# Performance work log

Hardware: AMD Instinct MI355X
Metric: run time of the kernel (lower is better)

Reference implementation:

```python
import jax, jax.numpy as jnp
import numpy as np

NUM_HEADS = 16
NUM_KV_HEADS = 4
HEAD_DIM = 128
HALF_DIM = HEAD_DIM // 2
LAMBDA_INIT = 0.8
LAMBDA_MIN = 0.0
LAMBDA_MAX = 1.0
CAUSAL = True
NORMALIZE_DIFF = True
NEG = -1.0e9


def setup_inputs() -> dict:
    key = jax.random.key(0)
    k1, k2, k3 = jax.random.split(key, 3)
    B, Sq, Sk = 1, 2048, 2048
    query = jax.random.normal(k1, (B, NUM_HEADS, Sq, HEAD_DIM), dtype=jnp.float32)
    key_t = jax.random.normal(k2, (B, NUM_KV_HEADS, Sk, HEAD_DIM), dtype=jnp.float32)
    value = jax.random.normal(k3, (B, NUM_KV_HEADS, Sk, HEAD_DIM), dtype=jnp.float32)
    return {"query": query, "key": key_t, "value": value}


def reference(query, key, value):
    scale = 1.0 / (HALF_DIM ** 0.5)
    lam = jnp.clip(jnp.float32(LAMBDA_INIT), LAMBDA_MIN, LAMBDA_MAX)
    # GQA: repeat KV heads to match query heads
    rep = NUM_HEADS // NUM_KV_HEADS
    k = jnp.repeat(key, rep, axis=1)    # [b,h,k,d]
    v = jnp.repeat(value, rep, axis=1)  # [b,h,k,d]
    q1, q2 = query[..., :HALF_DIM], query[..., HALF_DIM:]
    k1, k2 = k[..., :HALF_DIM], k[..., HALF_DIM:]
    scores1 = jnp.einsum('bhqd,bhkd->bhqk', q1, k1) * scale
    scores2 = jnp.einsum('bhqd,bhkd->bhqk', q2, k2) * scale
    if CAUSAL:
        Sq, Sk = query.shape[2], k.shape[2]
        mask = jnp.tril(jnp.ones((Sq, Sk), dtype=jnp.float32))  # lower-triangular causal
        scores1 = scores1 * mask + (1.0 - mask) * NEG
        scores2 = scores2 * mask + (1.0 - mask) * NEG
    attn1 = jax.nn.softmax(scores1, axis=-1)
    attn2 = jax.nn.softmax(scores2, axis=-1)
    diff_attn = attn1 - lam * attn2
    out = jnp.einsum('bhqk,bhkd->bhqd', diff_attn, v)
    if NORMALIZE_DIFF:
        out = out * (1.0 - LAMBDA_INIT)
    return out
```

## Files before the change

kernel.cpp:

```cpp
#include <hip/hip_runtime.h>

#define NUM_HEADS 16
#define HEAD_DIM  128
#define SEQ       2048
#define KT_STRIDE 8192

typedef __attribute__((ext_vector_type(8))) unsigned short us8;
typedef __attribute__((ext_vector_type(8))) __bf16 bf16x8;
typedef __attribute__((ext_vector_type(4))) float f32x4;
typedef __attribute__((ext_vector_type(16))) float f32x16;
typedef __attribute__((ext_vector_type(4))) unsigned u32x4;

static __device__ inline unsigned short f2bf(float x) {
    union { float f; unsigned u; } v; v.f = x;
    unsigned r = v.u + 0x7FFFu + ((v.u >> 16) & 1u);
    return (unsigned short)(r >> 16);
}
static __device__ inline unsigned pk2bf(float a, float b) {
    return (unsigned)f2bf(a) | ((unsigned)f2bf(b) << 16);
}
static __device__ inline float fast_exp2(float x) {
#if __has_builtin(__builtin_amdgcn_exp2f)
    return __builtin_amdgcn_exp2f(x);
#else
    return exp2f(x);
#endif
}
static __device__ inline unsigned pack_hi(unsigned clo, unsigned chi) {
#if __has_builtin(__builtin_amdgcn_perm)
    return __builtin_amdgcn_perm(chi, clo, 0x07060302u);
#else
    return (clo >> 16) | (chi & 0xffff0000u);
#endif
}
static __device__ inline f32x16 mfma32(us8 a, us8 b, f32x16 c) {
    return __builtin_amdgcn_mfma_f32_32x32x16_bf16(
        __builtin_bit_cast(bf16x8, a), __builtin_bit_cast(bf16x8, b), c, 0, 0, 0);
}

__global__ __launch_bounds__(256)
void prep_frag(const float* __restrict__ K, const float* __restrict__ V,
               unsigned short* __restrict__ KF, unsigned short* __restrict__ VF)
{
    const int bx  = (int)blockIdx.x, t = (int)threadIdx.x;
    const int which = bx & 1, kt = (bx >> 1) & 31, kvh = bx >> 6;
    __shared__ __align__(16) float Ls[64][132];

    const float* src = (which ? V : K) + ((size_t)kvh * SEQ + kt * 64) * HEAD_DIM;
    #pragma unroll
    for (int i = 0; i < 8; ++i) {
        const int idx = t + i * 256;
        const int r = idx >> 5, c4 = idx & 31;
        *(float4*)&Ls[r][c4 * 4] = *(const float4*)(src + (size_t)r * HEAD_DIM + c4 * 4);
    }
    __syncthreads();

    if (!which) {
        #pragma unroll
        for (int i = 0; i < 4; ++i) {
            const int c = t + i * 256;
            const int lane = c & 63, ds = (c >> 6) & 3, mat = (c >> 8) & 1, kh = c >> 9;
            const int H = lane >> 5;
            const int row = kh * 32 + (lane & 31);
            const int dim = mat * 64 + ds * 16 + H * 8;
            u32x4 pk;
            #pragma unroll
            for (int jj = 0; jj < 4; ++jj)
                pk[jj] = pk2bf(Ls[row][dim + 2*jj], Ls[row][dim + 2*jj + 1]);
            *(us8*)(KF + ((size_t)(kvh * 32 + kt) * 16 + kh * 8 + mat * 4 + ds) * 512 + lane * 8)
                = __builtin_bit_cast(us8, pk);
        }
    } else {
        #pragma unroll
        for (int i = 0; i < 4; ++i) {
            const int c = t + i * 256;
            const int lane = c & 63, db = (c >> 6) & 3, ks = (c >> 8) & 1, kh = c >> 9;
            const int H = lane >> 5;
            const int s0 = kh * 32 + ks * 16 + H * 8;
            const int d  = db * 32 + (lane & 31);
            u32x4 pk;
            #pragma unroll
            for (int jj = 0; jj < 4; ++jj)
                pk[jj] = pk2bf(Ls[s0 + 2*jj][d], Ls[s0 + 2*jj + 1][d]);
            *(us8*)(VF + ((size_t)(kvh * 32 + kt) * 16 + kh * 8 + ks * 4 + db) * 512 + lane * 8)
                = __builtin_bit_cast(us8, pk);
        }
    }
}

__global__ __launch_bounds__(256, 2)
void diff_attn_mfma10(const float* __restrict__ Q,
                      const unsigned short* __restrict__ KF,
                      const unsigned short* __restrict__ VF,
                      float* __restrict__ Out)
{
    __shared__ float cb[2][32][136];
    __shared__ float rsb[2][2][32];

    const int t   = (int)threadIdx.x;
    const int wv  = t >> 6;
    const int ln  = t & 63;
    const int mat = wv >> 1;
    const int kh  = wv & 1;
    const int q   = ln & 31;
    const int H   = ln >> 5;

    const int bx   = (int)blockIdx.x;
    const int h    = bx & 15;
    const int idx  = bx >> 4;
    const int qtA  = idx, qtB = 63 - idx;
    const int nktA = (qtA >> 1) + 1;
    const int kvh  = h >> 2;

    const unsigned short* kfb = KF + ((size_t)kvh * 32 * 16 + kh * 8 + mat * 4) * 512 + ln * 8;
    const unsigned short* vfb = VF + ((size_t)kvh * 32 * 16 + kh * 8) * 512 + ln * 8;

    const float qscale = 0.125f * 1.44269504088896340736f;

    us8 qhi[4];
    auto loadQ = [&](int q0c) {
        const float* qr = Q + ((size_t)h * SEQ + q0c + q) * HEAD_DIM + mat * 64;
        #pragma unroll
        for (int ds = 0; ds < 4; ++ds) {
            const int d0 = ds * 16 + H * 8;
            float x[8];
            *(float4*)&x[0] = *(const float4*)(qr + d0);
            *(float4*)&x[4] = *(const float4*)(qr + d0 + 4);
            us8 hi8;
            #pragma unroll
            for (int j = 0; j < 8; ++j) hi8[j] = f2bf(x[j] * qscale);
            qhi[ds] = hi8;
        }
    };

    f32x16 o[4];
    f32x4  rsv;

    auto epilogue = [&](int q0c) {
        __syncthreads();
        float rsc = (rsv[0] + rsv[1]) + (rsv[2] + rsv[3]);
        rsc += __shfl_xor(rsc, 32, 64);
        if (ln < 32) rsb[mat][kh][ln] = rsc;
        if (kh == 1) {
            #pragma unroll
            for (int db = 0; db < 4; ++db)
                #pragma unroll
                for (int i = 0; i < 4; ++i) {
                    float4 v = { o[db][i*4+0], o[db][i*4+1], o[db][i*4+2], o[db][i*4+3] };
                    *(float4*)&cb[mat][q][db * 32 + 8 * i + 4 * H] = v;
                }
        }
        __syncthreads();
        if (kh == 0) {
            const float l = rsb[mat][0][q] + rsb[mat][1][q];
            const float a = mat ? (0.16f / l) : (0.2f / l);
            #pragma unroll
            for (int db = 0; db < 4; ++db)
                #pragma unroll
                for (int i = 0; i < 4; ++i) {
                    float4 v = *(float4*)&cb[mat][q][db * 32 + 8 * i + 4 * H];
                    o[db][i*4+0] = (o[db][i*4+0] + v.x) * a;
                    o[db][i*4+1] = (o[db][i*4+1] + v.y) * a;
                    o[db][i*4+2] = (o[db][i*4+2] + v.z) * a;
                    o[db][i*4+3] = (o[db][i*4+3] + v.w) * a;
                }
            if (mat == 1) {
                #pragma unroll
                for (int db = 0; db < 4; ++db)
                    #pragma unroll
                    for (int i = 0; i < 4; ++i) {
                        float4 v = { o[db][i*4+0], o[db][i*4+1], o[db][i*4+2], o[db][i*4+3] };
                        *(float4*)&cb[1][q][db * 32 + 8 * i + 4 * H] = v;
                    }
            }
        }
        __syncthreads();
        if (wv == 0) {
            float* ob = Out + ((size_t)h * SEQ + q0c + q) * HEAD_DIM;
            #pragma unroll
            for (int db = 0; db < 4; ++db)
                #pragma unroll
                for (int i = 0; i < 4; ++i) {
                    float4 v = *(float4*)&cb[1][q][db * 32 + 8 * i + 4 * H];
                    float4 r;
                    r.x = o[db][i*4+0] - v.x;
                    r.y = o[db][i*4+1] - v.y;
                    r.z = o[db][i*4+2] - v.z;
                    r.w = o[db][i*4+3] - v.w;
                    *(float4*)(ob + db * 32 + 8 * i + 4 * H) = r;
                }
        }
    };

    auto run_seg = [&](int q0c, int nseg) {
        us8 kaA[4], kaB[4];

        auto body = [&](int j, us8 (&kaIn)[4], us8 (&kaOut)[4], f32x16& sIn, f32x16& sOut) {
            us8 va[8];
            {
                const unsigned short* vb = vfb + (size_t)j * KT_STRIDE;
                #pragma unroll
                for (int c = 0; c < 8; ++c) va[c] = *(const us8*)(vb + c * 512);
            }
            if (j + 2 < nseg) {
                const unsigned short* kb = kfb + (size_t)(j + 2) * KT_STRIDE;
                #pragma unroll
                for (int ds = 0; ds < 4; ++ds) kaOut[ds] = *(const us8*)(kb + ds * 512);
            }
            sOut = (f32x16)0.f;
            if (j + 1 < nseg) {
                #pragma unroll
                for (int ds = 0; ds < 4; ++ds) sOut = mfma32(kaIn[ds], qhi[ds], sOut);
            }
            unsigned c[16];
            if (j == nseg - 1) {
                const int kg0 = j * 64 + kh * 32 + 4 * H;
                const int qg  = q0c + q;
                #pragma unroll
                for (int r = 0; r < 16; ++r) {
                    const int kg = kg0 + (r & 3) + ((r >> 2) << 3);
                    float e = (kg <= qg) ? fast_exp2(sIn[r]) : 0.f;
                    c[r] = __builtin_bit_cast(unsigned, e);
                }
            } else {
                #pragma unroll
                for (int r = 0; r < 16; ++r)
                    c[r] = __builtin_bit_cast(unsigned, fast_exp2(sIn[r]));
            }
            #pragma unroll
            for (int ks = 0; ks < 2; ++ks) {
                const unsigned pA = pack_hi(c[8*ks+0], c[8*ks+1]);
                const unsigned pB = pack_hi(c[8*ks+2], c[8*ks+3]);
                const unsigned pC = pack_hi(c[8*ks+4], c[8*ks+5]);
                const unsigned pD = pack_hi(c[8*ks+6], c[8*ks+7]);
                rsv[0] += __builtin_bit_cast(float, pA << 16);
                rsv[1] += __builtin_bit_cast(float, pA & 0xffff0000u);
                rsv[2] += __builtin_bit_cast(float, pB << 16);
                rsv[3] += __builtin_bit_cast(float, pB & 0xffff0000u);
                rsv[0] += __builtin_bit_cast(float, pC << 16);
                rsv[1] += __builtin_bit_cast(float, pC & 0xffff0000u);
                rsv[2] += __builtin_bit_cast(float, pD << 16);
                rsv[3] += __builtin_bit_cast(float, pD & 0xffff0000u);
                const unsigned x1 = H ? pA : pC;
                const unsigned x2 = H ? pB : pD;
                const unsigned t1 = (unsigned)__shfl_xor((int)x1, 32, 64);
                const unsigned t2 = (unsigned)__shfl_xor((int)x2, 32, 64);
                u32x4 bw;
                bw[0] = H ? t1 : pA;
                bw[1] = H ? t2 : pB;
                bw[2] = H ? pC : t1;
                bw[3] = H ? pD : t2;
                const us8 bp = __builtin_bit_cast(us8, bw);
                #pragma unroll
                for (int db = 0; db < 4; ++db)
                    o[db] = mfma32(va[ks * 4 + db], bp, o[db]);
            }
        };

        f32x16 s0, s1;
        #pragma unroll
        for (int ds = 0; ds < 4; ++ds) kaA[ds] = *(const us8*)(kfb + ds * 512);
        s0 = (f32x16)0.f;
        #pragma unroll
        for (int ds = 0; ds < 4; ++ds) s0 = mfma32(kaA[ds], qhi[ds], s0);
        if (nseg > 1) {
            #pragma unroll
            for (int ds = 0; ds < 4; ++ds) kaA[ds] = *(const us8*)(kfb + KT_STRIDE + ds * 512);
        }

        int j = 0;
        for (; j + 2 <= nseg; j += 2) {
            body(j,     kaA, kaB, s0, s1);
            body(j + 1, kaB, kaA, s1, s0);
        }
        if (j < nseg) body(j, kaA, kaB, s0, s1);
    };

    loadQ(qtA * 32);
    #pragma unroll
    for (int i = 0; i < 4; ++i) o[i] = (f32x16)0.f;
    rsv = (f32x4)0.f;
    run_seg(qtA * 32, nktA);
    epilogue(qtA * 32);

    loadQ(qtB * 32);
    #pragma unroll
    for (int i = 0; i < 4; ++i) o[i] = (f32x16)0.f;
    rsv = (f32x4)0.f;
    run_seg(qtB * 32, 33 - nktA);
    epilogue(qtB * 32);
}

extern "C" void kernel_launch(void* const* d_in, const int* in_sizes, int n_in,
                              void* d_out, int out_size, void* d_ws, size_t ws_size,
                              hipStream_t stream) {
    const float* Q = (const float*)d_in[0];
    const float* K = (const float*)d_in[1];
    const float* V = (const float*)d_in[2];
    float* Out = (float*)d_out;

    unsigned short* KF = (unsigned short*)d_ws;
    unsigned short* VF = KF + (size_t)4 * SEQ * HEAD_DIM;

    prep_frag<<<256, 256, 0, stream>>>(K, V, KF, VF);
    diff_attn_mfma10<<<512, 256, 0, stream>>>(Q, KF, VF, Out);
}
```

Baseline: 111.9 us.

## Use one query tile per block with heavy-first ordering and raised occupancy

Replaces the paired-tile scheme, where each block processed query tiles idx and 63-idx, with one 32-row query tile per block. The grid doubles to 1024, with tiles ordered longest-first so the causal imbalance is handled by the scheduler. Launch bounds rise from 2 to 3 blocks per SM. To fit the register budget, the S-score software pipeline is dropped (QK^T is now computed in the same iteration) and the V fragment loads are split into two halves. The cost is less latency hiding inside each wave, which is expected to be offset by more resident waves.

```diff
diff --git a/kernel.cpp b/kernel.cpp
--- a/kernel.cpp
+++ b/kernel.cpp
@@ -88,8 +88,8 @@
     }
 }
 
-__global__ __launch_bounds__(256, 2)
-void diff_attn_mfma10(const float* __restrict__ Q,
+__global__ __launch_bounds__(256, 3)
+void diff_attn_mfma11(const float* __restrict__ Q,
                       const unsigned short* __restrict__ KF,
                       const unsigned short* __restrict__ VF,
                       float* __restrict__ Out)
@@ -107,9 +107,9 @@
 
     const int bx   = (int)blockIdx.x;
     const int h    = bx & 15;
-    const int idx  = bx >> 4;
-    const int qtA  = idx, qtB = 63 - idx;
-    const int nktA = (qtA >> 1) + 1;
+    const int qt   = 63 - (bx >> 4);
+    const int nkt  = (qt >> 1) + 1;
+    const int q0   = qt * 32;
     const int kvh  = h >> 2;
 
     const unsigned short* kfb = KF + ((size_t)kvh * 32 * 16 + kh * 8 + mat * 4) * 512 + ln * 8;
@@ -118,8 +118,8 @@
     const float qscale = 0.125f * 1.44269504088896340736f;
 
     us8 qhi[4];
-    auto loadQ = [&](int q0c) {
-        const float* qr = Q + ((size_t)h * SEQ + q0c + q) * HEAD_DIM + mat * 64;
+    {
+        const float* qr = Q + ((size_t)h * SEQ + q0 + q) * HEAD_DIM + mat * 64;
         #pragma unroll
         for (int ds = 0; ds < 4; ++ds) {
             const int d0 = ds * 16 + H * 8;
@@ -131,164 +131,142 @@
             for (int j = 0; j < 8; ++j) hi8[j] = f2bf(x[j] * qscale);
             qhi[ds] = hi8;
         }
+    }
+
+    f32x16 o[4];
+    f32x4  rsv = (f32x4)0.f;
+    #pragma unroll
+    for (int i = 0; i < 4; ++i) o[i] = (f32x16)0.f;
+
+    auto body = [&](int j, us8 (&kaIn)[4], us8 (&kaOut)[4]) {
+        us8 va0[4];
+        {
+            const unsigned short* vb = vfb + (size_t)j * KT_STRIDE;
+            #pragma unroll
+            for (int c = 0; c < 4; ++c) va0[c] = *(const us8*)(vb + c * 512);
+        }
+        if (j + 1 < nkt) {
+            const unsigned short* kb = kfb + (size_t)(j + 1) * KT_STRIDE;
+            #pragma unroll
+            for (int ds = 0; ds < 4; ++ds) kaOut[ds] = *(const us8*)(kb + ds * 512);
+        }
+        f32x16 s = (f32x16)0.f;
+        #pragma unroll
+        for (int ds = 0; ds < 4; ++ds) s = mfma32(kaIn[ds], qhi[ds], s);
+        unsigned c[16];
+        if (j == nkt - 1) {
+            const int kg0 = j * 64 + kh * 32 + 4 * H;
+            const int qg  = q0 + q;
+            #pragma unroll
+            for (int r = 0; r < 16; ++r) {
+                const int kg = kg0 + (r & 3) + ((r >> 2) << 3);
+                float e = (kg <= qg) ? fast_exp2(s[r]) : 0.f;
+                c[r] = __builtin_bit_cast(unsigned, e);
+            }
+        } else {
+            #pragma unroll
+            for (int r = 0; r < 16; ++r)
+                c[r] = __builtin_bit_cast(unsigned, fast_exp2(s[r]));
+        }
+        us8 va1[4];
+        #pragma unroll
+        for (int ks = 0; ks < 2; ++ks) {
+            const unsigned pA = pack_hi(c[8*ks+0], c[8*ks+1]);
+            const unsigned pB = pack_hi(c[8*ks+2], c[8*ks+3]);
+            const unsigned pC = pack_hi(c[8*ks+4], c[8*ks+5]);
+            const unsigned pD = pack_hi(c[8*ks+6], c[8*ks+7]);
+            rsv[0] += __builtin_bit_cast(float, pA << 16);
+            rsv[1] += __builtin_bit_cast(float, pA & 0xffff0000u);
+            rsv[2] += __builtin_bit_cast(float, pB << 16);
+            rsv[3] += __builtin_bit_cast(float, pB & 0xffff0000u);
+            rsv[0] += __builtin_bit_cast(float, pC << 16);
+            rsv[1] += __builtin_bit_cast(float, pC & 0xffff0000u);
+            rsv[2] += __builtin_bit_cast(float, pD << 16);
+            rsv[3] += __builtin_bit_cast(float, pD & 0xffff0000u);
+            if (ks == 0) {
+                const unsigned short* vb = vfb + (size_t)j * KT_STRIDE + 4 * 512;
+                #pragma unroll
+                for (int c2 = 0; c2 < 4; ++c2) va1[c2] = *(const us8*)(vb + c2 * 512);
+            }
+            const unsigned x1 = H ? pA : pC;
+            const unsigned x2 = H ? pB : pD;
+            const unsigned t1 = (unsigned)__shfl_xor((int)x1, 32, 64);
+            const unsigned t2 = (unsigned)__shfl_xor((int)x2, 32, 64);
+            u32x4 bw;
+            bw[0] = H ? t1 : pA;
+            bw[1] = H ? t2 : pB;
+            bw[2] = H ? pC : t1;
+            bw[3] = H ? pD : t2;
+            const us8 bp = __builtin_bit_cast(us8, bw);
+            #pragma unroll
+            for (int db = 0; db < 4; ++db)
+                o[db] = mfma32(ks ? va1[db] : va0[db], bp, o[db]);
+        }
     };
 
-    f32x16 o[4];
-    f32x4  rsv;
-
-    auto epilogue = [&](int q0c) {
-        __syncthreads();
-        float rsc = (rsv[0] + rsv[1]) + (rsv[2] + rsv[3]);
-        rsc += __shfl_xor(rsc, 32, 64);
-        if (ln < 32) rsb[mat][kh][ln] = rsc;
-        if (kh == 1) {
+    us8 kaA[4], kaB[4];
+    #pragma unroll
+    for (int ds = 0; ds < 4; ++ds) kaA[ds] = *(const us8*)(kfb + ds * 512);
+    int j = 0;
+    for (; j + 2 <= nkt; j += 2) {
+        body(j,     kaA, kaB);
+        body(j + 1, kaB, kaA);
+    }
+    if (j < nkt) body(j, kaA, kaB);
+
+    __syncthreads();
+    float rsc = (rsv[0] + rsv[1]) + (rsv[2] + rsv[3]);
+    rsc += __shfl_xor(rsc, 32, 64);
+    if (ln < 32) rsb[mat][kh][ln] = rsc;
+    if (kh == 1) {
+        #pragma unroll
+        for (int db = 0; db < 4; ++db)
+            #pragma unroll
+            for (int i = 0; i < 4; ++i) {
+                float4 v = { o[db][i*4+0], o[db][i*4+1], o[db][i*4+2], o[db][i*4+3] };
+                *(float4*)&cb[mat][q][db * 32 + 8 * i + 4 * H] = v;
+            }
+    }
+    __syncthreads();
+    if (kh == 0) {
+        const float l = rsb[mat][0][q] + rsb[mat][1][q];
+        const float a = mat ? (0.16f / l) : (0.2f / l);
+        #pragma unroll
+        for (int db = 0; db < 4; ++db)
+            #pragma unroll
+            for (int i = 0; i < 4; ++i) {
+                float4 v = *(float4*)&cb[mat][q][db * 32 + 8 * i + 4 * H];
+                o[db][i*4+0] = (o[db][i*4+0] + v.x) * a;
+                o[db][i*4+1] = (o[db][i*4+1] + v.y) * a;
+                o[db][i*4+2] = (o[db][i*4+2] + v.z) * a;
+                o[db][i*4+3] = (o[db][i*4+3] + v.w) * a;
+            }
+        if (mat == 1) {
             #pragma unroll
             for (int db = 0; db < 4; ++db)
                 #pragma unroll
                 for (int i = 0; i < 4; ++i) {
                     float4 v = { o[db][i*4+0], o[db][i*4+1], o[db][i*4+2], o[db][i*4+3] };
-                    *(float4*)&cb[mat][q][db * 32 + 8 * i + 4 * H] = v;
+                    *(float4*)&cb[1][q][db * 32 + 8 * i + 4 * H] = v;
                 }
         }
-        __syncthreads();
-        if (kh == 0) {
-            const float l = rsb[mat][0][q] + rsb[mat][1][q];
-            const float a = mat ? (0.16f / l) : (0.2f / l);
-            #pragma unroll
-            for (int db = 0; db < 4; ++db)
-                #pragma unroll
-                for (int i = 0; i < 4; ++i) {
-                    float4 v = *(float4*)&cb[mat][q][db * 32 + 8 * i + 4 * H];
-                    o[db][i*4+0] = (o[db][i*4+0] + v.x) * a;
-                    o[db][i*4+1] = (o[db][i*4+1] + v.y) * a;
-                    o[db][i*4+2] = (o[db][i*4+2] + v.z) * a;
-                    o[db][i*4+3] = (o[db][i*4+3] + v.w) * a;
-                }
-            if (mat == 1) {
-                #pragma unroll
-                for (int db = 0; db < 4; ++db)
-                    #pragma unroll
-                    for (int i = 0; i < 4; ++i) {
-                        float4 v = { o[db][i*4+0], o[db][i*4+1], o[db][i*4+2], o[db][i*4+3] };
-                        *(float4*)&cb[1][q][db * 32 + 8 * i + 4 * H] = v;
-                    }
-            }
-        }
-        __syncthreads();
-        if (wv == 0) {
-            float* ob = Out + ((size_t)h * SEQ + q0c + q) * HEAD_DIM;
-            #pragma unroll
-            for (int db = 0; db < 4; ++db)
-                #pragma unroll
-                for (int i = 0; i < 4; ++i) {
-                    float4 v = *(float4*)&cb[1][q][db * 32 + 8 * i + 4 * H];
-                    float4 r;
-                    r.x = o[db][i*4+0] - v.x;
-                    r.y = o[db][i*4+1] - v.y;
-                    r.z = o[db][i*4+2] - v.z;
-                    r.w = o[db][i*4+3] - v.w;
-                    *(float4*)(ob + db * 32 + 8 * i + 4 * H) = r;
-                }
-        }
-    };
-
-    auto run_seg = [&](int q0c, int nseg) {
-        us8 kaA[4], kaB[4];
-
-        auto body = [&](int j, us8 (&kaIn)[4], us8 (&kaOut)[4], f32x16& sIn, f32x16& sOut) {
-            us8 va[8];
-            {
-                const unsigned short* vb = vfb + (size_t)j * KT_STRIDE;
-                #pragma unroll
-                for (int c = 0; c < 8; ++c) va[c] = *(const us8*)(vb + c * 512);
-            }
-            if (j + 2 < nseg) {
-                const unsigned short* kb = kfb + (size_t)(j + 2) * KT_STRIDE;
-                #pragma unroll
-                for (int ds = 0; ds < 4; ++ds) kaOut[ds] = *(const us8*)(kb + ds * 512);
-            }
-            sOut = (f32x16)0.f;
-            if (j + 1 < nseg) {
-                #pragma unroll
-                for (int ds = 0; ds < 4; ++ds) sOut = mfma32(kaIn[ds], qhi[ds], sOut);
-            }
-            unsigned c[16];
-            if (j == nseg - 1) {
-                const int kg0 = j * 64 + kh * 32 + 4 * H;
-                const int qg  = q0c + q;
-                #pragma unroll
-                for (int r = 0; r < 16; ++r) {
-                    const int kg = kg0 + (r & 3) + ((r >> 2) << 3);
-                    float e = (kg <= qg) ? fast_exp2(sIn[r]) : 0.f;
-                    c[r] = __builtin_bit_cast(unsigned, e);
-                }
-            } else {
-                #pragma unroll
-                for (int r = 0; r < 16; ++r)
-                    c[r] = __builtin_bit_cast(unsigned, fast_exp2(sIn[r]));
-            }
-            #pragma unroll
-            for (int ks = 0; ks < 2; ++ks) {
-                const unsigned pA = pack_hi(c[8*ks+0], c[8*ks+1]);
-                const unsigned pB = pack_hi(c[8*ks+2], c[8*ks+3]);
-                const unsigned pC = pack_hi(c[8*ks+4], c[8*ks+5]);
-                const unsigned pD = pack_hi(c[8*ks+6], c[8*ks+7]);
-                rsv[0] += __builtin_bit_cast(float, pA << 16);
-                rsv[1] += __builtin_bit_cast(float, pA & 0xffff0000u);
-                rsv[2] += __builtin_bit_cast(float, pB << 16);
-                rsv[3] += __builtin_bit_cast(float, pB & 0xffff0000u);
-                rsv[0] += __builtin_bit_cast(float, pC << 16);
-                rsv[1] += __builtin_bit_cast(float, pC & 0xffff0000u);
-                rsv[2] += __builtin_bit_cast(float, pD << 16);
-                rsv[3] += __builtin_bit_cast(float, pD & 0xffff0000u);
-                const unsigned x1 = H ? pA : pC;
-                const unsigned x2 = H ? pB : pD;
-                const unsigned t1 = (unsigned)__shfl_xor((int)x1, 32, 64);
-                const unsigned t2 = (unsigned)__shfl_xor((int)x2, 32, 64);
-                u32x4 bw;
-                bw[0] = H ? t1 : pA;
-                bw[1] = H ? t2 : pB;
-                bw[2] = H ? pC : t1;
-                bw[3] = H ? pD : t2;
-                const us8 bp = __builtin_bit_cast(us8, bw);
-                #pragma unroll
-                for (int db = 0; db < 4; ++db)
-                    o[db] = mfma32(va[ks * 4 + db], bp, o[db]);
-            }
-        };
-
-        f32x16 s0, s1;
-        #pragma unroll
-        for (int ds = 0; ds < 4; ++ds) kaA[ds] = *(const us8*)(kfb + ds * 512);
-        s0 = (f32x16)0.f;
-        #pragma unroll
-        for (int ds = 0; ds < 4; ++ds) s0 = mfma32(kaA[ds], qhi[ds], s0);
-        if (nseg > 1) {
-            #pragma unroll
-            for (int ds = 0; ds < 4; ++ds) kaA[ds] = *(const us8*)(kfb + KT_STRIDE + ds * 512);
-        }
-
-        int j = 0;
-        for (; j + 2 <= nseg; j += 2) {
-            body(j,     kaA, kaB, s0, s1);
-            body(j + 1, kaB, kaA, s1, s0);
-        }
-        if (j < nseg) body(j, kaA, kaB, s0, s1);
-    };
-
-    loadQ(qtA * 32);
-    #pragma unroll
-    for (int i = 0; i < 4; ++i) o[i] = (f32x16)0.f;
-    rsv = (f32x4)0.f;
-    run_seg(qtA * 32, nktA);
-    epilogue(qtA * 32);
-
-    loadQ(qtB * 32);
-    #pragma unroll
-    for (int i = 0; i < 4; ++i) o[i] = (f32x16)0.f;
-    rsv = (f32x4)0.f;
-    run_seg(qtB * 32, 33 - nktA);
-    epilogue(qtB * 32);
+    }
+    __syncthreads();
+    if (wv == 0) {
+        float* ob = Out + ((size_t)h * SEQ + q0 + q) * HEAD_DIM;
+        #pragma unroll
+        for (int db = 0; db < 4; ++db)
+            #pragma unroll
+            for (int i = 0; i < 4; ++i) {
+                float4 v = *(float4*)&cb[1][q][db * 32 + 8 * i + 4 * H];
+                float4 r;
+                r.x = o[db][i*4+0] - v.x;
+                r.y = o[db][i*4+1] - v.y;
+                r.z = o[db][i*4+2] - v.z;
+                r.w = o[db][i*4+3] - v.w;
+                *(float4*)(ob + db * 32 + 8 * i + 4 * H) = r;
+            }
+    }
 }
 
 extern "C" void kernel_launch(void* const* d_in, const int* in_sizes, int n_in,
@@ -303,5 +281,5 @@
     unsigned short* VF = KF + (size_t)4 * SEQ * HEAD_DIM;
 
     prep_frag<<<256, 256, 0, stream>>>(K, V, KF, VF);
-    diff_attn_mfma10<<<512, 256, 0, stream>>>(Q, KF, VF, Out);
-}
+    diff_attn_mfma11<<<1024, 256, 0, stream>>>(Q, KF, VF, Out);
+}
```

Measured after the change: 139.3 us. 24.5% more time.

## Stage V tiles in double-buffered LDS via global_load_lds shared across waves

Applied to the files above, without the earlier changes.

V fragments are now brought into a two-slot LDS buffer with asynchronous global_load_lds, one tile ahead. All four waves read them from LDS instead of each wave loading its own copy from global memory. This removes the duplicate V loads between the two waves that share a K half and overlaps the next tile's transfer with current compute. In exchange it adds a block-wide barrier every iteration, one more at the end of the epilogue, and about 32KB of extra LDS per block, which could serialize waves that were previously free-running.

```diff
diff --git a/kernel.cpp b/kernel.cpp
--- a/kernel.cpp
+++ b/kernel.cpp
@@ -4,6 +4,7 @@
 #define HEAD_DIM  128
 #define SEQ       2048
 #define KT_STRIDE 8192
+#define VBYTES    16384
 
 typedef __attribute__((ext_vector_type(8))) unsigned short us8;
 typedef __attribute__((ext_vector_type(8))) __bf16 bf16x8;
@@ -89,11 +90,12 @@
 }
 
 __global__ __launch_bounds__(256, 2)
-void diff_attn_mfma10(const float* __restrict__ Q,
+void diff_attn_mfma12(const float* __restrict__ Q,
                       const unsigned short* __restrict__ KF,
                       const unsigned short* __restrict__ VF,
                       float* __restrict__ Out)
 {
+    __shared__ __align__(16) unsigned char vbuf[2][VBYTES];
     __shared__ float cb[2][32][136];
     __shared__ float rsb[2][2][32];
 
@@ -113,7 +115,7 @@
     const int kvh  = h >> 2;
 
     const unsigned short* kfb = KF + ((size_t)kvh * 32 * 16 + kh * 8 + mat * 4) * 512 + ln * 8;
-    const unsigned short* vfb = VF + ((size_t)kvh * 32 * 16 + kh * 8) * 512 + ln * 8;
+    const unsigned short* vfbase = VF + (size_t)kvh * 32 * KT_STRIDE;
 
     const float qscale = 0.125f * 1.44269504088896340736f;
 
@@ -130,6 +132,18 @@
             #pragma unroll
             for (int j = 0; j < 8; ++j) hi8[j] = f2bf(x[j] * qscale);
             qhi[ds] = hi8;
+        }
+    };
+
+    auto issueV = [&](int j, int p) {
+        const unsigned short* src = vfbase + (size_t)j * KT_STRIDE;
+        #pragma unroll
+        for (int i = 0; i < 4; ++i) {
+            const int off = i * 256 + wv * 64;
+            __builtin_amdgcn_global_load_lds(
+                (const __attribute__((address_space(1))) unsigned*)(src + (size_t)(off + ln) * 8),
+                (__attribute__((address_space(3))) unsigned*)(&vbuf[p][(size_t)off * 16]),
+                16, 0, 0);
         }
     };
 
@@ -190,18 +204,16 @@
                     *(float4*)(ob + db * 32 + 8 * i + 4 * H) = r;
                 }
         }
+        __syncthreads();
     };
 
     auto run_seg = [&](int q0c, int nseg) {
         us8 kaA[4], kaB[4];
 
-        auto body = [&](int j, us8 (&kaIn)[4], us8 (&kaOut)[4], f32x16& sIn, f32x16& sOut) {
-            us8 va[8];
-            {
-                const unsigned short* vb = vfb + (size_t)j * KT_STRIDE;
-                #pragma unroll
-                for (int c = 0; c < 8; ++c) va[c] = *(const us8*)(vb + c * 512);
-            }
+        auto body = [&](int j, int cur, us8 (&kaIn)[4], us8 (&kaOut)[4],
+                        f32x16& sIn, f32x16& sOut) {
+            __syncthreads();
+            if (j + 1 < nseg) issueV(j + 1, cur ^ 1);
             if (j + 2 < nseg) {
                 const unsigned short* kb = kfb + (size_t)(j + 2) * KT_STRIDE;
                 #pragma unroll
@@ -212,6 +224,10 @@
                 #pragma unroll
                 for (int ds = 0; ds < 4; ++ds) sOut = mfma32(kaIn[ds], qhi[ds], sOut);
             }
+            us8 va[8];
+            #pragma unroll
+            for (int c2 = 0; c2 < 8; ++c2)
+                va[c2] = *(const us8*)(&vbuf[cur][(size_t)((kh * 8 + c2) * 64 + ln) * 16]);
             unsigned c[16];
             if (j == nseg - 1) {
                 const int kg0 = j * 64 + kh * 32 + 4 * H;
@@ -257,6 +273,7 @@
             }
         };
 
+        issueV(0, 0);
         f32x16 s0, s1;
         #pragma unroll
         for (int ds = 0; ds < 4; ++ds) kaA[ds] = *(const us8*)(kfb + ds * 512);
@@ -270,10 +287,10 @@
 
         int j = 0;
         for (; j + 2 <= nseg; j += 2) {
-            body(j,     kaA, kaB, s0, s1);
-            body(j + 1, kaB, kaA, s1, s0);
-        }
-        if (j < nseg) body(j, kaA, kaB, s0, s1);
+            body(j,     0, kaA, kaB, s0, s1);
+            body(j + 1, 1, kaB, kaA, s1, s0);
+        }
+        if (j < nseg) body(j, j & 1, kaA, kaB, s0, s1);
     };
 
     loadQ(qtA * 32);
@@ -303,5 +320,5 @@
     unsigned short* VF = KF + (size_t)4 * SEQ * HEAD_DIM;
 
     prep_frag<<<256, 256, 0, stream>>>(K, V, KF, VF);
-    diff_attn_mfma10<<<512, 256, 0, stream>>>(Q, KF, VF, Out);
-}
+    diff_attn_mfma12<<<512, 256, 0, stream>>>(Q, KF, VF, Out);
+}
```

After: 114.1 us. About the same (+2.0%).
